# Optimization experiments

Measured on AMD Instinct MI355X. Metric: run time of the kernel, lower is better.

The kernel has to match this reference:

```python
import jax, jax.numpy as jnp
import numpy as np

H_HEADS = 32
KV_HEADS = 8
HEAD_DIM = 128
HIDDEN = 2048
EPS = 1e-6


def rms_norm(x, w):
    # normalize over last dim (head_dim)
    var = jnp.mean(jnp.square(x), axis=-1, keepdims=True)
    return x * jax.lax.rsqrt(var + EPS) * w


def rotate_half(x):
    x1, x2 = jnp.split(x, 2, axis=-1)
    return jnp.concatenate([-x2, x1], axis=-1)


def setup_inputs() -> dict:
    key = jax.random.key(0)
    ks = jax.random.split(key, 8)
    B, Q, CTX = 1, 1024, 2048
    T = CTX + Q
    hidden_states = jax.random.normal(ks[0], (B, Q, HIDDEN), jnp.float32)
    target_hidden = jax.random.normal(ks[1], (B, CTX, HIDDEN), jnp.float32)
    # RoPE tables over the full concatenated length
    inv_freq = 1.0 / (10000.0 ** (np.arange(0, HEAD_DIM, 2, dtype=np.float32) / HEAD_DIM))
    pos = np.arange(T, dtype=np.float32)
    freqs = np.outer(pos, inv_freq)                     # [T, hd/2]
    emb = np.concatenate([freqs, freqs], axis=-1)       # [T, hd]
    cos = jnp.asarray(np.cos(emb))[None]                # [1, T, hd]
    sin = jnp.asarray(np.sin(emb))[None]
    # custom mask: context fully visible, causal within noise block
    noise_causal = jnp.tril(jnp.ones((Q, Q), bool))
    mask = jnp.concatenate([jnp.ones((Q, CTX), bool), noise_causal], axis=1)
    attention_mask = mask[None, None]                   # [1,1,Q,T]
    scale = 0.02
    wq = jax.random.normal(ks[2], (H_HEADS * HEAD_DIM, HIDDEN), jnp.float32) * scale
    wk = jax.random.normal(ks[3], (KV_HEADS * HEAD_DIM, HIDDEN), jnp.float32) * scale
    wv = jax.random.normal(ks[4], (KV_HEADS * HEAD_DIM, HIDDEN), jnp.float32) * scale
    wo = jax.random.normal(ks[5], (HIDDEN, H_HEADS * HEAD_DIM), jnp.float32) * scale
    q_norm_w = jnp.ones((HEAD_DIM,), jnp.float32)
    k_norm_w = jnp.ones((HEAD_DIM,), jnp.float32)
    return {"hidden_states": hidden_states, "target_hidden": target_hidden,
            "cos": cos, "sin": sin, "attention_mask": attention_mask,
            "wq": wq, "wk": wk, "wv": wv, "wo": wo,
            "q_norm_w": q_norm_w, "k_norm_w": k_norm_w}


def reference(hidden_states, target_hidden, cos, sin, attention_mask,
              wq, wk, wv, wo, q_norm_w, k_norm_w):
    B, Q, _ = hidden_states.shape
    CTX = target_hidden.shape[1]
    T = CTX + Q
    n_rep = H_HEADS // KV_HEADS
    scaling = HEAD_DIM ** -0.5

    # Q from noise tokens, QK-RMSNorm per head
    q = (hidden_states @ wq.T).reshape(B, Q, H_HEADS, HEAD_DIM)
    q = rms_norm(q, q_norm_w).transpose(0, 2, 1, 3)          # [B,H,Q,hd]

    # K/V: context then noise, concatenated along sequence
    k = jnp.concatenate([target_hidden @ wk.T, hidden_states @ wk.T], axis=1)
    k = rms_norm(k.reshape(B, T, KV_HEADS, HEAD_DIM), k_norm_w).transpose(0, 2, 1, 3)  # [B,Hk,T,hd]
    v = jnp.concatenate([target_hidden @ wv.T, hidden_states @ wv.T], axis=1)
    v = v.reshape(B, T, KV_HEADS, HEAD_DIM).transpose(0, 2, 1, 3)                       # [B,Hk,T,hd]

    # offset RoPE: K uses all T positions, Q uses the last Q positions
    cos_b = cos[:, None]                                      # [B,1,T,hd]
    sin_b = sin[:, None]
    q = q * cos_b[:, :, -Q:, :] + rotate_half(q) * sin_b[:, :, -Q:, :]
    k = k * cos_b + rotate_half(k) * sin_b

    # GQA attention without materializing repeated K/V
    qg = q.reshape(B, KV_HEADS, n_rep, Q, HEAD_DIM)
    scores = jnp.einsum('bgrqd,bgtd->bgrqt', qg, k) * scaling  # [B,Hk,rep,Q,T]
    scores = jnp.where(attention_mask[:, :, None], scores, jnp.finfo(scores.dtype).min)
    probs = jax.nn.softmax(scores, axis=-1)
    out = jnp.einsum('bgrqt,bgtd->bgrqd', probs, v)            # [B,Hk,rep,Q,hd]
    out = out.reshape(B, H_HEADS, Q, HEAD_DIM).transpose(0, 2, 1, 3).reshape(B, Q, H_HEADS * HEAD_DIM)
    return out @ wo.T
```

## Files before the change

kernel.cpp:

```cpp
#include <hip/hip_runtime.h>

#define HIDDEN 2048
#define NQ     1024
#define NCTX   2048
#define NTOT   3072
#define NHEADS 32
#define KVH    8
#define HD     128

typedef __attribute__((ext_vector_type(8))) __bf16 bf16x8;
typedef __attribute__((ext_vector_type(4))) __bf16 bf16x4;
typedef __attribute__((ext_vector_type(4))) float  f32x4;

#define MFMA16(a, b, c) __builtin_amdgcn_mfma_f32_16x16x32_bf16(a, b, c, 0, 0, 0)

#define MSTATIC 12.0f

__device__ __forceinline__ void load_lds16(const void* g, void* l) {
    __builtin_amdgcn_global_load_lds(
        (const __attribute__((address_space(1))) unsigned int*)g,
        (__attribute__((address_space(3))) unsigned int*)l, 16, 0, 0);
}

__global__ __launch_bounds__(256) void conv4_f32_bf16(const float* __restrict__ s0,
                                                      __bf16* __restrict__ d0, int n0,
                                                      const float* __restrict__ s1,
                                                      __bf16* __restrict__ d1, int n1,
                                                      const float* __restrict__ s2,
                                                      __bf16* __restrict__ d2, int n2,
                                                      const float* __restrict__ s3,
                                                      __bf16* __restrict__ d3, int n3) {
    const float* s; __bf16* d; int n;
    switch (blockIdx.y) {
        case 0:  s = s0; d = d0; n = n0; break;
        case 1:  s = s1; d = d1; n = n1; break;
        case 2:  s = s2; d = d2; n = n2; break;
        default: s = s3; d = d3; n = n3; break;
    }
    int i = blockIdx.x * 256 + threadIdx.x;
    int stride = gridDim.x * 256;
    for (; i < n; i += stride) {
        float4 v = ((const float4*)s)[i];
        bf16x4 o;
        o[0] = (__bf16)v.x; o[1] = (__bf16)v.y;
        o[2] = (__bf16)v.z; o[3] = (__bf16)v.w;
        ((bf16x4*)d)[i] = o;
    }
}

__device__ __forceinline__ void gemm_compute256(const __bf16 (&As)[256][64],
                                                const __bf16 (&Bs)[64][64],
                                                f32x4 (&acc)[4][4],
                                                int wm, int n16, int quad, int rx) {
#pragma unroll
    for (int ks = 0; ks < 2; ks++) {
        bf16x8 af[4], bfr[4];
#pragma unroll
        for (int i = 0; i < 4; i++)
            af[i] = *(const bf16x8*)&As[wm + i * 16 + n16][((ks * 4 + quad) ^ rx) * 8];
#pragma unroll
        for (int j = 0; j < 4; j++)
            bfr[j] = *(const bf16x8*)&Bs[j * 16 + n16][((ks * 4 + quad) ^ rx) * 8];
#pragma unroll
        for (int i = 0; i < 4; i++)
#pragma unroll
            for (int j = 0; j < 4; j++)
                acc[i][j] = MFMA16(af[i], bfr[j], acc[i][j]);
    }
}

template <typename OutT>
__device__ __forceinline__ void gemm_epi256(const f32x4 (&acc)[4][4],
                                            OutT* __restrict__ Cblk, int ldc,
                                            int wm, int n16, int quad) {
#pragma unroll
    for (int i = 0; i < 4; i++)
#pragma unroll
        for (int j = 0; j < 4; j++)
#pragma unroll
            for (int r = 0; r < 4; r++)
                Cblk[(long)(wm + i * 16 + quad * 4 + r) * ldc + j * 16 + n16] =
                    (OutT)acc[i][j][r];
}

template <typename OutT>
__device__ __forceinline__ void gemm25664_bb(__bf16 (&As)[256][64], __bf16 (&Bs)[64][64],
                                             const __bf16* __restrict__ Ablk,
                                             const __bf16* __restrict__ Bblk,
                                             OutT* __restrict__ Cblk,
                                             int K, int lda, int ldb, int ldc) {
    const int tid  = threadIdx.x;
    const int lane = tid & 63;
    const int w    = tid >> 6;
    const int n16  = lane & 15;
    const int quad = lane >> 4;
    const int wm   = w * 64;

    f32x4 acc[4][4];
    const f32x4 fzero = {0.f, 0.f, 0.f, 0.f};
#pragma unroll
    for (int i = 0; i < 4; i++)
#pragma unroll
        for (int j = 0; j < 4; j++) acc[i][j] = fzero;

    const int arow  = w * 64 + (lane >> 3);
    const int brow  = w * 16 + (lane >> 3);
    const int sxor  = (lane >> 3) & 7;
    const int scol  = (lane & 7) * 8;
    const int sgcol = ((lane & 7) ^ sxor) * 8;
    const __bf16* Ap = Ablk + (long)arow * lda + sgcol;
    const __bf16* Bp = Bblk + (long)brow * ldb + sgcol;
    const int rx = n16 & 7;

    for (int k0 = 0; k0 < K; k0 += 64) {
#pragma unroll
        for (int i = 0; i < 8; i++)
            load_lds16(Ap + (long)i * 8 * lda + k0, &As[arow + i * 8][scol]);
#pragma unroll
        for (int i = 0; i < 2; i++)
            load_lds16(Bp + (long)i * 8 * ldb + k0, &Bs[brow + i * 8][scol]);
        __syncthreads();
        gemm_compute256(As, Bs, acc, wm, n16, quad, rx);
        __syncthreads();
    }
    gemm_epi256(acc, Cblk, ldc, wm, n16, quad);
}

template <typename OutT>
__device__ __forceinline__ void gemm25664_fb(__bf16 (&As)[256][64], __bf16 (&Bs)[64][64],
                                             const __bf16* __restrict__ Ablk,
                                             const float* __restrict__ Bblk,
                                             OutT* __restrict__ Cblk,
                                             int K, int lda, int ldb, int ldc) {
    const int tid  = threadIdx.x;
    const int lane = tid & 63;
    const int w    = tid >> 6;
    const int n16  = lane & 15;
    const int quad = lane >> 4;
    const int wm   = w * 64;

    f32x4 acc[4][4];
    const f32x4 fzero = {0.f, 0.f, 0.f, 0.f};
#pragma unroll
    for (int i = 0; i < 4; i++)
#pragma unroll
        for (int j = 0; j < 4; j++) acc[i][j] = fzero;

    const int arow  = w * 64 + (lane >> 3);
    const int sxor  = (lane >> 3) & 7;
    const int scol  = (lane & 7) * 8;
    const int sgcol = ((lane & 7) ^ sxor) * 8;
    const __bf16* Ap = Ablk + (long)arow * lda + sgcol;

    const int brr  = tid >> 2;
    const int bc0  = (tid & 3) * 16;
    const int bch  = (tid & 3) * 2;
    const int bxor = brr & 7;
    const float* Bptr = Bblk + (long)brr * ldb + bc0;

    const int rx = n16 & 7;
    float4 breg[4];

#define LOAD_B(kk)                                                             \
    _Pragma("unroll") for (int i = 0; i < 4; i++)                              \
        breg[i] = *(const float4*)(Bptr + (kk) + i * 4);

    LOAD_B(0);
    for (int k0 = 0; k0 < K; k0 += 64) {
#pragma unroll
        for (int i = 0; i < 8; i++)
            load_lds16(Ap + (long)i * 8 * lda + k0, &As[arow + i * 8][scol]);
        {
            bf16x8 b0, b1;
#pragma unroll
            for (int j = 0; j < 4; j++) {
                b0[j]     = (__bf16)breg[0][j]; b0[j + 4] = (__bf16)breg[1][j];
                b1[j]     = (__bf16)breg[2][j]; b1[j + 4] = (__bf16)breg[3][j];
            }
            *(bf16x8*)&Bs[brr][((bch + 0) ^ bxor) * 8] = b0;
            *(bf16x8*)&Bs[brr][((bch + 1) ^ bxor) * 8] = b1;
        }
        if (k0 + 64 < K) LOAD_B(k0 + 64);
        __syncthreads();
        gemm_compute256(As, Bs, acc, wm, n16, quad, rx);
        __syncthreads();
    }
#undef LOAD_B
    gemm_epi256(acc, Cblk, ldc, wm, n16, quad);
}

__global__ __launch_bounds__(256, 4) void gemm_kvq(const __bf16* __restrict__ tgtb,
                                                   const __bf16* __restrict__ hidb,
                                                   const __bf16* __restrict__ wkb,
                                                   const __bf16* __restrict__ wvb,
                                                   const float* __restrict__ wq,
                                                   __bf16* __restrict__ kbf,
                                                   __bf16* __restrict__ vbf,
                                                   __bf16* __restrict__ qbf) {
    __shared__ __bf16 As[256][64];
    __shared__ __bf16 Bs[64][64];
    const int bid = blockIdx.x;
    const int b = (bid & 7) * 80 + (bid >> 3);
    if (b < 384) {
        const int z = b >= 192, t = b - z * 192;
        const int m0 = (t >> 4) * 256, n0 = (t & 15) * 64;
        const __bf16* Ap = (m0 < 2048) ? tgtb + (long)m0 * 2048
                                       : hidb + (long)(m0 - 2048) * 2048;
        const __bf16* Bp = (z ? wvb : wkb) + (long)n0 * 2048;
        __bf16* Cp = (z ? vbf : kbf) + (long)m0 * 1024 + n0;
        gemm25664_bb<__bf16>(As, Bs, Ap, Bp, Cp, 2048, 2048, 2048, 1024);
    } else {
        const int t = b - 384;
        const int m0 = (t >> 6) * 256, n0 = (t & 63) * 64;
        gemm25664_fb<__bf16>(As, Bs, hidb + (long)m0 * 2048, wq + (long)n0 * 2048,
                             qbf + (long)m0 * 4096 + n0, 2048, 2048, 2048, 4096);
    }
}

__global__ __launch_bounds__(256, 4) void gemm_wo4(const __bf16* __restrict__ A,
                                                   const float* __restrict__ wo,
                                                   float* __restrict__ out,
                                                   float* __restrict__ p1,
                                                   float* __restrict__ p2,
                                                   float* __restrict__ p3) {
    __shared__ __bf16 As[256][64];
    __shared__ __bf16 Bs[64][64];
    const int bid = blockIdx.x;
    const int b = (bid & 7) * 64 + (bid >> 3);
    const int z = b >> 7, t = b & 127;
    const int m0 = (t >> 5) * 256, n0 = (t & 31) * 64;
    float* C;
    switch (z) {
        case 0:  C = out; break;
        case 1:  C = p1;  break;
        case 2:  C = p2;  break;
        default: C = p3;  break;
    }
    gemm25664_fb<float>(As, Bs, A + (long)m0 * 4096 + z * 1024,
                        wo + (long)n0 * 4096 + z * 1024,
                        C + (long)m0 * 2048 + n0, 1024, 4096, 4096, 2048);
}

__global__ __launch_bounds__(256) void add4_wo(float* __restrict__ out,
                                               const float* __restrict__ p1,
                                               const float* __restrict__ p2,
                                               const float* __restrict__ p3, int n4) {
    int i = blockIdx.x * 256 + threadIdx.x;
    int stride = gridDim.x * 256;
    for (; i < n4; i += stride) {
        float4 a = ((const float4*)out)[i];
        float4 b = ((const float4*)p1)[i];
        float4 c = ((const float4*)p2)[i];
        float4 d = ((const float4*)p3)[i];
        float4 o;
        o.x = (a.x + b.x) + (c.x + d.x);
        o.y = (a.y + b.y) + (c.y + d.y);
        o.z = (a.z + b.z) + (c.z + d.z);
        o.w = (a.w + b.w) + (c.w + d.w);
        ((float4*)out)[i] = o;
    }
}

__global__ __launch_bounds__(256) void rmsnorm_rope2(__bf16* __restrict__ xq,
                                                     const float* __restrict__ wq,
                                                     __bf16* __restrict__ xk,
                                                     const float* __restrict__ wk,
                                                     const float* __restrict__ cosb,
                                                     const float* __restrict__ sinb) {
    const int z = blockIdx.y;
    __bf16*      x = z ? xk : xq;
    const float* w = z ? wk : wq;
    const int nheads     = z ? 8 : 32;
    const int row_stride = z ? 1024 : 4096;
    const int pos_offset = z ? 0 : 2048;
    const float outscale = z ? 1.0f : 0.08838834764831845f;
    const int nitems     = z ? 3072 * 8 : 1024 * 32;

    int item = blockIdx.x * 4 + (threadIdx.x >> 6);
    int lane = threadIdx.x & 63;
    if (item >= nitems) return;
    int row = item / nheads;
    int head = item - row * nheads;
    __bf16* p = x + (long)row * row_stride + head * HD;

    float x1 = (float)p[lane], x2 = (float)p[lane + 64];
    float ss = x1 * x1 + x2 * x2;
#pragma unroll
    for (int o = 32; o >= 1; o >>= 1) ss += __shfl_xor(ss, o);
    float r = rsqrtf(ss * (1.0f / 128.0f) + 1e-6f) * outscale;

    int pos = pos_offset + row;
    float c1 = cosb[pos * HD + lane], c2 = cosb[pos * HD + lane + 64];
    float s1 = sinb[pos * HD + lane], s2 = sinb[pos * HD + lane + 64];
    float y1 = x1 * r * w[lane];
    float y2 = x2 * r * w[lane + 64];
    p[lane]      = (__bf16)(y1 * c1 - y2 * s1);
    p[lane + 64] = (__bf16)(y2 * c2 + y1 * s2);
}

__global__ __launch_bounds__(256) void transpose_v(const __bf16* __restrict__ v,
                                                   __bf16* __restrict__ vt) {
    __shared__ __bf16 T[64][68];
    const int tid = threadIdx.x;
    const int t0 = blockIdx.x * 64;
    const int d0 = blockIdx.y * 64;
    const int g  = blockIdx.z;
    const __bf16* src = v + (long)t0 * 1024 + g * 128 + d0;
#pragma unroll
    for (int i = 0; i < 4; i++) {
        int idx = tid + i * 256;
        int r = idx >> 4, c4 = (idx & 15) * 4;
        *(bf16x4*)&T[r][c4] = *(const bf16x4*)(src + (long)r * 1024 + c4);
    }
    __syncthreads();
    __bf16* dst = vt + (long)g * 128 * 3072 + (long)d0 * 3072 + t0;
#pragma unroll
    for (int i = 0; i < 4; i++) {
        int idx = tid + i * 256;
        int r = idx >> 4, c4 = (idx & 15) * 4;
        bf16x4 o;
        o[0] = T[c4 + 0][r]; o[1] = T[c4 + 1][r];
        o[2] = T[c4 + 2][r]; o[3] = T[c4 + 3][r];
        *(bf16x4*)(dst + (long)r * 3072 + c4) = o;
    }
}

__global__ __launch_bounds__(256) void flash_attn_splitk(const __bf16* __restrict__ qb,
                                                         const __bf16* __restrict__ kb,
                                                         const __bf16* __restrict__ vtg,
                                                         __bf16* __restrict__ Opart0,
                                                         __bf16* __restrict__ Opart1,
                                                         float* __restrict__ lsum) {
    __shared__ __bf16 KsU[64 * 136];
    __shared__ __bf16 Vs[128][72];
#define KS(r, c) KsU[(r) * 136 + (c)]
#define PS(w_, m_, t_) KsU[(w_) * 2176 + (m_) * 68 + (t_)]

    const int tid  = threadIdx.x;
    const int lane = tid & 63;
    const int w    = tid >> 6;
    const int n    = lane & 15;
    const int quad = lane >> 4;

    const int bid = blockIdx.x;
    const int s   = blockIdx.y;
    const int g  = bid & 7;
    const int jj = bid >> 3;
    const int h  = g * 4 + (jj & 3);
    const int qt = jj >> 2;

    const int qr0 = qt * 128 + w * 16;

    bf16x8 qf[2][4];
#pragma unroll
    for (int mt = 0; mt < 2; mt++) {
        const __bf16* qp = qb + (long)(qr0 + mt * 64 + n) * 4096 + h * 128 + quad * 8;
        qf[mt][0] = *(const bf16x8*)(qp);
        qf[mt][1] = *(const bf16x8*)(qp + 32);
        qf[mt][2] = *(const bf16x8*)(qp + 64);
        qf[mt][3] = *(const bf16x8*)(qp + 96);
    }

    f32x4 O[2][8];
    const f32x4 fzero = {0.f, 0.f, 0.f, 0.f};
#pragma unroll
    for (int mt = 0; mt < 2; mt++)
#pragma unroll
        for (int dt = 0; dt < 8; dt++) O[mt][dt] = fzero;
    float l_loc[2] = {0.f, 0.f};

    const int ntot = 34 + 2 * qt;
    const int half = ntot >> 1;
    const int tbeg = s ? half : 0;
    const int tend = s ? ntot : half;

    const int krr = tid >> 4, kc8 = (tid & 15) * 8;
    const int vrr = tid >> 3, vc8 = (tid & 7) * 8;
    const __bf16* kp = kb + g * 128 + (long)(tbeg * 64 + krr) * 1024 + kc8;
    const __bf16* vp = vtg + (long)g * 128 * 3072 + (long)vrr * 3072 + tbeg * 64 + vc8;

    for (int tt = tbeg; tt < tend; tt++) {
#pragma unroll
        for (int i = 0; i < 4; i++)
            *(bf16x8*)&KS(krr + i * 16, kc8) = *(const bf16x8*)(kp + (long)i * 16 * 1024);
#pragma unroll
        for (int i = 0; i < 4; i++)
            *(bf16x8*)&Vs[vrr + i * 32][vc8] = *(const bf16x8*)(vp + (long)i * 32 * 3072);
        kp += 64 * 1024;
        vp += 64;
        __syncthreads();

        f32x4 S[2][4];
#pragma unroll
        for (int nt = 0; nt < 4; nt++) {
            f32x4 a0 = fzero, a1 = fzero;
#pragma unroll
            for (int ks = 0; ks < 4; ks++) {
                bf16x8 kf = *(const bf16x8*)&KS(nt * 16 + n, ks * 32 + quad * 8);
                a0 = MFMA16(kf, qf[0][ks], a0);
                a1 = MFMA16(kf, qf[1][ks], a1);
            }
            S[0][nt] = a0;
            S[1][nt] = a1;
        }

        if (tt >= ntot - 2) {
            const int t0 = tt * 64;
#pragma unroll
            for (int mt = 0; mt < 2; mt++) {
                const int lim = 2048 + qr0 + mt * 64 + n;
#pragma unroll
                for (int nt = 0; nt < 4; nt++)
#pragma unroll
                    for (int r = 0; r < 4; r++) {
                        int t = t0 + nt * 16 + quad * 4 + r;
                        if (t > lim) S[mt][nt][r] = -1e30f;
                    }
            }
        }

        __syncthreads();

#pragma unroll
        for (int mt = 0; mt < 2; mt++)
#pragma unroll
            for (int nt = 0; nt < 4; nt++)
#pragma unroll
                for (int r = 0; r < 4; r++) {
                    float p = __expf(S[mt][nt][r] - MSTATIC);
                    S[mt][nt][r] = p;
                    l_loc[mt] += p;
                }

#pragma unroll
        for (int mt = 0; mt < 2; mt++)
#pragma unroll
            for (int nt = 0; nt < 4; nt++) {
                bf16x4 pk;
#pragma unroll
                for (int r = 0; r < 4; r++) pk[r] = (__bf16)S[mt][nt][r];
                *(bf16x4*)&PS(w, mt * 16 + n, nt * 16 + quad * 4) = pk;
            }

        bf16x8 pa[2][2];
#pragma unroll
        for (int mt = 0; mt < 2; mt++)
#pragma unroll
            for (int kg = 0; kg < 2; kg++)
                pa[mt][kg] = *(const bf16x8*)&PS(w, mt * 16 + n, kg * 32 + quad * 8);

#pragma unroll
        for (int dt = 0; dt < 8; dt++) {
            bf16x8 vf0 = *(const bf16x8*)&Vs[dt * 16 + n][quad * 8];
            bf16x8 vf1 = *(const bf16x8*)&Vs[dt * 16 + n][32 + quad * 8];
#pragma unroll
            for (int mt = 0; mt < 2; mt++) {
                f32x4 acc = O[mt][dt];
                acc = MFMA16(pa[mt][0], vf0, acc);
                acc = MFMA16(pa[mt][1], vf1, acc);
                O[mt][dt] = acc;
            }
        }
        __syncthreads();
    }

#pragma unroll
    for (int mt = 0; mt < 2; mt++) {
        float sm = l_loc[mt];
        sm += __shfl_xor(sm, 16);
        sm += __shfl_xor(sm, 32);
        l_loc[mt] = sm;
    }

    __bf16* Op = s ? Opart1 : Opart0;
    const long tb = (long)(h * 8 + qt) * 128 * 128;
#pragma unroll
    for (int mt = 0; mt < 2; mt++)
#pragma unroll
        for (int dt = 0; dt < 8; dt++)
#pragma unroll
            for (int r = 0; r < 4; r++)
                Op[tb + (long)(mt * 64 + w * 16 + quad * 4 + r) * 128 + dt * 16 + n] =
                    (__bf16)O[mt][dt][r];
    if (quad == 0) {
        const int lb = (s * 256 + h * 8 + qt) * 128 + w * 16;
#pragma unroll
        for (int mt = 0; mt < 2; mt++)
            lsum[lb + mt * 64 + n] = l_loc[mt];
    }
#undef KS
#undef PS
}

__global__ __launch_bounds__(256) void flash_merge(const __bf16* __restrict__ O0,
                                                   const __bf16* __restrict__ O1,
                                                   const float* __restrict__ lsum,
                                                   __bf16* __restrict__ ob) {
    const int bx = blockIdx.x;
    const int h   = bx >> 4;
    const int r6  = bx & 15;
    const int qt  = r6 >> 1;
    const int sub = r6 & 1;
    const int row  = threadIdx.x >> 2;
    const int cseg = (threadIdx.x & 3) * 32;
    const int mrow = sub * 64 + row;

    const int tilei = h * 8 + qt;
    float inv = 1.0f / (lsum[tilei * 128 + mrow] + lsum[(256 + tilei) * 128 + mrow]);

    const long src = (long)tilei * 128 * 128 + (long)mrow * 128 + cseg;
    __bf16* dst = ob + (long)(qt * 128 + mrow) * 4096 + h * 128 + cseg;
#pragma unroll
    for (int j = 0; j < 4; j++) {
        bf16x8 x0 = *(const bf16x8*)(O0 + src + j * 8);
        bf16x8 x1 = *(const bf16x8*)(O1 + src + j * 8);
        bf16x8 o;
#pragma unroll
        for (int k = 0; k < 8; k++)
            o[k] = (__bf16)(((float)x0[k] + (float)x1[k]) * inv);
        *(bf16x8*)(dst + j * 8) = o;
    }
}

extern "C" void kernel_launch(void* const* d_in, const int* in_sizes, int n_in,
                              void* d_out, int out_size, void* d_ws, size_t ws_size,
                              hipStream_t stream) {
    const float* hidden = (const float*)d_in[0];
    const float* target = (const float*)d_in[1];
    const float* cosb   = (const float*)d_in[2];
    const float* sinb   = (const float*)d_in[3];
    const float* wq = (const float*)d_in[5];
    const float* wk = (const float*)d_in[6];
    const float* wv = (const float*)d_in[7];
    const float* wo = (const float*)d_in[8];
    const float* qw = (const float*)d_in[9];
    const float* kw = (const float*)d_in[10];
    float* out = (float*)d_out;

    char* ws = (char*)d_ws;
    const long MB = 1 << 20;
    __bf16* hidb = (__bf16*)(ws);
    __bf16* tgtb = (__bf16*)(ws + 4 * MB);
    __bf16* wkb  = (__bf16*)(ws + 12 * MB);
    __bf16* wvb  = (__bf16*)(ws + 16 * MB);
    __bf16* kbf  = (__bf16*)(ws + 20 * MB);
    __bf16* vbf  = (__bf16*)(ws + 26 * MB);
    __bf16* vtg  = (__bf16*)(ws + 32 * MB);
    float*  lbuf = (float*)(ws);
    __bf16* Op0  = (__bf16*)(ws + 4 * MB);
    __bf16* Op1  = (__bf16*)(ws + 12 * MB);
    __bf16* attnb= (__bf16*)(ws + 20 * MB);
    float*  po1  = (float*)(ws + 4 * MB);
    float*  po2  = (float*)(ws + 12 * MB);
    float*  po3  = (float*)(ws + 28 * MB);
    __bf16* qbf  = (__bf16*)d_out;

    dim3 blk(256);

    conv4_f32_bf16<<<dim3(1024, 4), blk, 0, stream>>>(
        hidden, hidb, (1024 * 2048) / 4, target, tgtb, (2048 * 2048) / 4,
        wk, wkb, (1024 * 2048) / 4, wv, wvb, (1024 * 2048) / 4);

    gemm_kvq<<<640, blk, 0, stream>>>(tgtb, hidb, wkb, wvb, wq, kbf, vbf, qbf);

    rmsnorm_rope2<<<dim3(8192, 2), blk, 0, stream>>>(qbf, qw, kbf, kw, cosb, sinb);

    transpose_v<<<dim3(48, 2, 8), blk, 0, stream>>>(vbf, vtg);

    flash_attn_splitk<<<dim3(256, 2), blk, 0, stream>>>(qbf, kbf, vtg, Op0, Op1, lbuf);
    flash_merge<<<512, blk, 0, stream>>>(Op0, Op1, lbuf, attnb);

    gemm_wo4<<<512, blk, 0, stream>>>(attnb, wo, out, po1, po2, po3);
    add4_wo<<<1024, blk, 0, stream>>>(out, po1, po2, po3, (1024 * 2048) / 4);
}
```

Baseline: 338.6 us.

## Split attention KV three ways and prefetch next KV tile into registers

The flash attention kernel now splits the key range into three parts instead of two, launching 768 blocks, and the merge kernel sums three partial outputs. K/V tiles are prefetched into registers one iteration ahead, and P gets its own shared buffer so one barrier per iteration can be dropped. The aim is better GPU occupancy and hiding global load latency behind MFMA work. The costs are more registers and LDS per block (launch_bounds now asks for 3 blocks per CU), extra partial-output traffic, and a reshuffled workspace layout.

```diff
diff --git a/kernel.cpp b/kernel.cpp
--- a/kernel.cpp
+++ b/kernel.cpp
@@ -325,16 +325,18 @@
     }
 }
 
-__global__ __launch_bounds__(256) void flash_attn_splitk(const __bf16* __restrict__ qb,
-                                                         const __bf16* __restrict__ kb,
-                                                         const __bf16* __restrict__ vtg,
-                                                         __bf16* __restrict__ Opart0,
-                                                         __bf16* __restrict__ Opart1,
-                                                         float* __restrict__ lsum) {
+__global__ __launch_bounds__(256, 3) void flash_attn_splitk(const __bf16* __restrict__ qb,
+                                                            const __bf16* __restrict__ kb,
+                                                            const __bf16* __restrict__ vtg,
+                                                            __bf16* __restrict__ Opart0,
+                                                            __bf16* __restrict__ Opart1,
+                                                            __bf16* __restrict__ Opart2,
+                                                            float* __restrict__ lsum) {
     __shared__ __bf16 KsU[64 * 136];
     __shared__ __bf16 Vs[128][72];
+    __shared__ __bf16 PsU[4 * 32 * 68];
 #define KS(r, c) KsU[(r) * 136 + (c)]
-#define PS(w_, m_, t_) KsU[(w_) * 2176 + (m_) * 68 + (t_)]
+#define PS(w_, m_, t_) PsU[(w_) * 2176 + (m_) * 68 + (t_)]
 
     const int tid  = threadIdx.x;
     const int lane = tid & 63;
@@ -370,24 +372,37 @@
     float l_loc[2] = {0.f, 0.f};
 
     const int ntot = 34 + 2 * qt;
-    const int half = ntot >> 1;
-    const int tbeg = s ? half : 0;
-    const int tend = s ? ntot : half;
+    const int tbeg = (s * ntot) / 3;
+    const int tend = ((s + 1) * ntot) / 3;
 
     const int krr = tid >> 4, kc8 = (tid & 15) * 8;
     const int vrr = tid >> 3, vc8 = (tid & 7) * 8;
     const __bf16* kp = kb + g * 128 + (long)(tbeg * 64 + krr) * 1024 + kc8;
     const __bf16* vp = vtg + (long)g * 128 * 3072 + (long)vrr * 3072 + tbeg * 64 + vc8;
 
+    bf16x8 kreg[4], vreg[4];
+#define LOADKV()                                                               \
+    do {                                                                       \
+        _Pragma("unroll") for (int i = 0; i < 4; i++) {                        \
+            kreg[i] = *(const bf16x8*)(kp + (long)i * 16 * 1024);              \
+            vreg[i] = *(const bf16x8*)(vp + (long)i * 32 * 3072);              \
+        }                                                                      \
+        kp += 64 * 1024;                                                       \
+        vp += 64;                                                              \
+    } while (0)
+#define WRITEKV()                                                              \
+    do {                                                                       \
+        _Pragma("unroll") for (int i = 0; i < 4; i++) {                        \
+            *(bf16x8*)&KS(krr + i * 16, kc8) = kreg[i];                        \
+            *(bf16x8*)&Vs[vrr + i * 32][vc8] = vreg[i];                        \
+        }                                                                      \
+    } while (0)
+
+    LOADKV();
+    WRITEKV();
+    if (tbeg + 1 < tend) LOADKV();
+
     for (int tt = tbeg; tt < tend; tt++) {
-#pragma unroll
-        for (int i = 0; i < 4; i++)
-            *(bf16x8*)&KS(krr + i * 16, kc8) = *(const bf16x8*)(kp + (long)i * 16 * 1024);
-#pragma unroll
-        for (int i = 0; i < 4; i++)
-            *(bf16x8*)&Vs[vrr + i * 32][vc8] = *(const bf16x8*)(vp + (long)i * 32 * 3072);
-        kp += 64 * 1024;
-        vp += 64;
         __syncthreads();
 
         f32x4 S[2][4];
@@ -419,8 +434,6 @@
             }
         }
 
-        __syncthreads();
-
 #pragma unroll
         for (int mt = 0; mt < 2; mt++)
 #pragma unroll
@@ -461,8 +474,15 @@
                 O[mt][dt] = acc;
             }
         }
+
         __syncthreads();
-    }
+        if (tt + 1 < tend) {
+            WRITEKV();
+            if (tt + 2 < tend) LOADKV();
+        }
+    }
+#undef LOADKV
+#undef WRITEKV
 
 #pragma unroll
     for (int mt = 0; mt < 2; mt++) {
@@ -472,7 +492,7 @@
         l_loc[mt] = sm;
     }
 
-    __bf16* Op = s ? Opart1 : Opart0;
+    __bf16* Op = (s == 0) ? Opart0 : (s == 1 ? Opart1 : Opart2);
     const long tb = (long)(h * 8 + qt) * 128 * 128;
 #pragma unroll
     for (int mt = 0; mt < 2; mt++)
@@ -494,6 +514,7 @@
 
 __global__ __launch_bounds__(256) void flash_merge(const __bf16* __restrict__ O0,
                                                    const __bf16* __restrict__ O1,
+                                                   const __bf16* __restrict__ O2,
                                                    const float* __restrict__ lsum,
                                                    __bf16* __restrict__ ob) {
     const int bx = blockIdx.x;
@@ -506,7 +527,8 @@
     const int mrow = sub * 64 + row;
 
     const int tilei = h * 8 + qt;
-    float inv = 1.0f / (lsum[tilei * 128 + mrow] + lsum[(256 + tilei) * 128 + mrow]);
+    float inv = 1.0f / (lsum[tilei * 128 + mrow] + lsum[(256 + tilei) * 128 + mrow] +
+                        lsum[(512 + tilei) * 128 + mrow]);
 
     const long src = (long)tilei * 128 * 128 + (long)mrow * 128 + cseg;
     __bf16* dst = ob + (long)(qt * 128 + mrow) * 4096 + h * 128 + cseg;
@@ -514,10 +536,11 @@
     for (int j = 0; j < 4; j++) {
         bf16x8 x0 = *(const bf16x8*)(O0 + src + j * 8);
         bf16x8 x1 = *(const bf16x8*)(O1 + src + j * 8);
+        bf16x8 x2 = *(const bf16x8*)(O2 + src + j * 8);
         bf16x8 o;
 #pragma unroll
         for (int k = 0; k < 8; k++)
-            o[k] = (__bf16)(((float)x0[k] + (float)x1[k]) * inv);
+            o[k] = (__bf16)((((float)x0[k] + (float)x1[k]) + (float)x2[k]) * inv);
         *(bf16x8*)(dst + j * 8) = o;
     }
 }
@@ -539,20 +562,21 @@
 
     char* ws = (char*)d_ws;
     const long MB = 1 << 20;
-    __bf16* hidb = (__bf16*)(ws);
-    __bf16* tgtb = (__bf16*)(ws + 4 * MB);
-    __bf16* wkb  = (__bf16*)(ws + 12 * MB);
-    __bf16* wvb  = (__bf16*)(ws + 16 * MB);
-    __bf16* kbf  = (__bf16*)(ws + 20 * MB);
-    __bf16* vbf  = (__bf16*)(ws + 26 * MB);
-    __bf16* vtg  = (__bf16*)(ws + 32 * MB);
-    float*  lbuf = (float*)(ws);
-    __bf16* Op0  = (__bf16*)(ws + 4 * MB);
-    __bf16* Op1  = (__bf16*)(ws + 12 * MB);
-    __bf16* attnb= (__bf16*)(ws + 20 * MB);
-    float*  po1  = (float*)(ws + 4 * MB);
-    float*  po2  = (float*)(ws + 12 * MB);
-    float*  po3  = (float*)(ws + 28 * MB);
+    __bf16* kbf  = (__bf16*)(ws);
+    __bf16* vtg  = (__bf16*)(ws + 6 * MB);
+    __bf16* vbf  = (__bf16*)(ws + 12 * MB);
+    __bf16* hidb = (__bf16*)(ws + 20 * MB);
+    __bf16* tgtb = (__bf16*)(ws + 24 * MB);
+    __bf16* wkb  = (__bf16*)(ws + 32 * MB);
+    __bf16* wvb  = (__bf16*)(ws + 36 * MB);
+    __bf16* Op0  = (__bf16*)(ws + 12 * MB);
+    __bf16* Op1  = (__bf16*)(ws + 20 * MB);
+    __bf16* Op2  = (__bf16*)(ws + 28 * MB);
+    float*  lbuf = (float*)(ws + 36 * MB);
+    __bf16* attnb= (__bf16*)(ws);
+    float*  po1  = (float*)(ws + 8 * MB);
+    float*  po2  = (float*)(ws + 16 * MB);
+    float*  po3  = (float*)(ws + 24 * MB);
     __bf16* qbf  = (__bf16*)d_out;
 
     dim3 blk(256);
@@ -567,8 +591,9 @@
 
     transpose_v<<<dim3(48, 2, 8), blk, 0, stream>>>(vbf, vtg);
 
-    flash_attn_splitk<<<dim3(256, 2), blk, 0, stream>>>(qbf, kbf, vtg, Op0, Op1, lbuf);
-    flash_merge<<<512, blk, 0, stream>>>(Op0, Op1, lbuf, attnb);
+    flash_attn_splitk<<<dim3(256, 3), blk, 0, stream>>>(qbf, kbf, vtg,
+                                                        Op0, Op1, Op2, lbuf);
+    flash_merge<<<512, blk, 0, stream>>>(Op0, Op1, Op2, lbuf, attnb);
 
     gemm_wo4<<<512, blk, 0, stream>>>(attnb, wo, out, po1, po2, po3);
     add4_wo<<<1024, blk, 0, stream>>>(out, po1, po2, po3, (1024 * 2048) / 4);
```

New measurement: 374.1 us. 1.1x slower.
